# Kernel tuning notes

Hardware: AMD Instinct MI355X
Metric: run time of the kernel (lower is better)

The kernel has to match this reference:

```python
import jax, jax.numpy as jnp
import numpy as np

D_MODEL = 128
N_HEADS = 8
N_POINTS = 8
MAX_RES = 10.0


def setup_inputs() -> dict:
    key = jax.random.key(0)
    ks = jax.random.split(key, 12)
    B, C, H, W = 4, D_MODEL, 128, 128
    nh, P = N_HEADS, N_POINTS
    inp = {
        'nbr_fea': jax.random.normal(ks[0], (B, C, H, W), jnp.float32),
        'ext_fea': jax.random.normal(ks[1], (B, C, H, W), jnp.float32),
        'flow': jax.random.normal(ks[2], (B, 2, H, W), jnp.float32) * 2.0,
        'W_off': jax.random.normal(ks[3], (C, nh * P * 2), jnp.float32) * 0.02,
        'b_off': jax.random.normal(ks[4], (nh * P * 2,), jnp.float32) * 0.02,
        'W_attn': jax.random.normal(ks[5], (C, nh * P), jnp.float32) * 0.02,
        'b_attn': jnp.zeros((nh * P,), jnp.float32),
        'W_val': jax.random.normal(ks[6], (C, C), jnp.float32) * (1.0 / np.sqrt(C)),
        'b_val': jnp.zeros((C,), jnp.float32),
        'W_out': jax.random.normal(ks[7], (C, C), jnp.float32) * (1.0 / np.sqrt(C)),
        'b_out': jnp.zeros((C,), jnp.float32),
    }
    return inp


def _bilinear_gather(value, loc, H, W):
    # value: (B, nh, HW, dh)  loc: (B, nh, Q, P, 2) normalized to [0,1]
    # grid_sample semantics: align_corners=False, zero padding
    B, nh, HW, dh = value.shape
    Q, P = loc.shape[2], loc.shape[3]
    x = loc[..., 0] * W - 0.5  # (B,nh,Q,P) pixel coords
    y = loc[..., 1] * H - 0.5
    x0 = jnp.floor(x)
    y0 = jnp.floor(y)
    wx = x - x0
    wy = y - y0
    out = jnp.zeros((B, nh, Q * P, dh), value.dtype)
    for dx, dy, wgt in ((0, 0, (1 - wx) * (1 - wy)), (1, 0, wx * (1 - wy)),
                        (0, 1, (1 - wx) * wy), (1, 1, wx * wy)):
        xi = x0 + dx
        yi = y0 + dy
        valid = (xi >= 0) & (xi < W) & (yi >= 0) & (yi < H)
        xi_c = jnp.clip(xi, 0, W - 1).astype(jnp.int32)
        yi_c = jnp.clip(yi, 0, H - 1).astype(jnp.int32)
        idx = (yi_c * W + xi_c).reshape(B, nh, Q * P, 1)
        g = jnp.take_along_axis(value, idx, axis=2)  # (B,nh,QP,dh)
        w_eff = (wgt * valid.astype(value.dtype)).reshape(B, nh, Q * P, 1)
        out = out + g * w_eff
    return out.reshape(B, nh, Q, P, dh)


def reference(nbr_fea, ext_fea, flow, W_off, b_off, W_attn, b_attn, W_val, b_val, W_out, b_out):
    B, C, H, W = nbr_fea.shape
    nh, P = N_HEADS, N_POINTS
    dh = C // nh
    Q = H * W
    # normalized reference points (pixel centers / extent)
    ys = (jnp.arange(H, dtype=jnp.float32) + 0.5) / H
    xs = (jnp.arange(W, dtype=jnp.float32) + 0.5) / W
    yy, xx = jnp.meshgrid(ys, xs, indexing='ij')
    ref = jnp.stack([xx, yy], -1).reshape(Q, 2)  # (Q,2)

    ext = ext_fea.transpose(0, 2, 3, 1).reshape(B, Q, C)
    # flow-guided sampling offsets (pixels), residue bounded by tanh
    off = MAX_RES * jnp.tanh(ext @ W_off + b_off)
    off = off.reshape(B, Q, nh, P, 2)
    flow_q = flow.transpose(0, 2, 3, 1).reshape(B, Q, 1, 1, 2)
    norm = jnp.array([W, H], jnp.float32)
    loc = ref[None, :, None, None, :] + (flow_q + off) / norm  # (B,Q,nh,P,2)

    attn = jax.nn.softmax((ext @ W_attn + b_attn).reshape(B, Q, nh, P), axis=-1)

    val = (nbr_fea.transpose(0, 2, 3, 1).reshape(B, Q, C) @ W_val + b_val)
    val = val.reshape(B, Q, nh, dh).transpose(0, 2, 1, 3)  # (B,nh,HW,dh)

    sampled = _bilinear_gather(val, loc.transpose(0, 2, 1, 3, 4), H, W)  # (B,nh,Q,P,dh)
    agg = jnp.einsum('bnqpd,bqnp->bqnd', sampled, attn).reshape(B, Q, C)
    out = agg @ W_out + b_out  # (B,Q,C)
    return out.reshape(B, H, W, C).transpose(0, 3, 1, 2)
```

## Files before the change

### kernel.cpp

```cpp
#include <hip/hip_runtime.h>
#include <math.h>

namespace {
constexpr int B   = 4;
constexpr int C   = 128;
constexpr int H   = 128;
constexpr int W   = 128;
constexpr int HWn = H * W;
constexpr int NH  = 8;
}

using short8 = __attribute__((ext_vector_type(8))) short;
using f32x4  = __attribute__((ext_vector_type(4))) float;

__device__ __forceinline__ float fast_tanh(float x) {
  float e = __expf(2.f * x);
  return 1.f - 2.f / (e + 1.f);
}
__device__ __forceinline__ unsigned f2bf(float f) {
  unsigned u = __float_as_uint(f);
  return (u + 0x7FFFu + ((u >> 16) & 1u)) >> 16;
}
__device__ __forceinline__ unsigned pack2bf(float a, float b) {
  return f2bf(a) | (f2bf(b) << 16);
}

__global__ __launch_bounds__(256) void prep_weights_kernel(
    const float* __restrict__ Woff, const float* __restrict__ Wattn,
    const float* __restrict__ Wval, const float* __restrict__ Wout,
    unsigned short* __restrict__ wcat_t, unsigned short* __restrict__ wval_t,
    unsigned short* __restrict__ wout_t) {
  int row = blockIdx.x * 256 + threadIdx.x;
  if (row >= 448) return;
  const float* src; int ldn; int col; unsigned short* dst;
  if (row < 192) {
    if (row < 128) { src = Woff; ldn = 128; col = row; }
    else           { src = Wattn; ldn = 64; col = row - 128; }
    dst = wcat_t + row * 128;
  } else if (row < 320) {
    src = Wval; ldn = 128; col = row - 192; dst = wval_t + (row - 192) * 128;
  } else {
    src = Wout; ldn = 128; col = row - 320; dst = wout_t + (row - 320) * 128;
  }
  for (int k0 = 0; k0 < 128; k0 += 8) {
    unsigned pk[4];
#pragma unroll
    for (int j = 0; j < 4; ++j)
      pk[j] = pack2bf(src[(k0 + 2 * j) * ldn + col],
                      src[(k0 + 2 * j + 1) * ldn + col]);
    *(uint4*)(dst + k0) = make_uint4(pk[0], pk[1], pk[2], pk[3]);
  }
}

__global__ __launch_bounds__(256) void gemm_kernel(
    const float* __restrict__ nbr, const float* __restrict__ ext,
    const unsigned short* __restrict__ wval_t,
    const float* __restrict__ bv,
    const unsigned short* __restrict__ wcat_t,
    const float* __restrict__ boff, const float* __restrict__ battn,
    unsigned short* __restrict__ val, float* __restrict__ proj) {
  __shared__ unsigned short a_s[64 * 152];
  __shared__ unsigned short b_s[192 * 40];
  const int t    = threadIdx.x;
  const int grp  = blockIdx.x >> 10;
  const int id   = blockIdx.x & 1023;
  const int b    = id >> 8;
  const int q0   = (id & 255) * 64;
  const int wv   = t >> 6;
  const int lane = t & 63;
  const int li   = lane & 15, quad = lane >> 4;

  const float* Ab = (grp ? ext : nbr) + (size_t)b * C * HWn + q0;
#pragma unroll
  for (int it = 0; it < 4; ++it) {
    int idx = t + 256 * it;
    int kp  = idx >> 4;
    int q4  = (idx & 15) * 4;
    float4 fa = *(const float4*)(Ab + (size_t)(2 * kp) * HWn + q4);
    float4 fb = *(const float4*)(Ab + (size_t)(2 * kp + 1) * HWn + q4);
    const float* pa = &fa.x; const float* pb = &fb.x;
#pragma unroll
    for (int j = 0; j < 4; ++j)
      *(unsigned*)&a_s[(q4 + j) * 152 + 2 * kp] = pack2bf(pa[j], pb[j]);
  }

  if (grp == 0) {
    f32x4 acc[8];
#pragma unroll
    for (int n = 0; n < 8; ++n) acc[n] = (f32x4){0.f, 0.f, 0.f, 0.f};

    for (int ck = 0; ck < 4; ++ck) {
      __syncthreads();
#pragma unroll
      for (int it = 0; it < 2; ++it) {
        int idx = t + 256 * it;
        int n = idx >> 2, seg = idx & 3;
        *(uint4*)&b_s[n * 40 + seg * 8] =
            *(const uint4*)(wval_t + n * 128 + ck * 32 + seg * 8);
      }
      __syncthreads();
      short8 af = *(const short8*)&a_s[(16 * wv + li) * 152 + ck * 32 + quad * 8];
#pragma unroll
      for (int n = 0; n < 8; ++n) {
        short8 bfr = *(const short8*)&b_s[(16 * n + li) * 40 + quad * 8];
        acc[n] = __builtin_amdgcn_mfma_f32_16x16x32_bf16(af, bfr, acc[n], 0, 0, 0);
      }
    }

    __syncthreads();
#pragma unroll
    for (int n = 0; n < 8; ++n) {
      float bias = bv[16 * n + li];
#pragma unroll
      for (int reg = 0; reg < 4; ++reg) {
        int q = 16 * wv + 4 * quad + reg;
        a_s[q * 152 + 16 * n + li] = (unsigned short)f2bf(acc[n][reg] + bias);
      }
    }
    __syncthreads();
    {
      const int qi = t & 63, r = t >> 6;
      uint4 v0 = *(const uint4*)&a_s[qi * 152 + 32 * r];
      uint4 v1 = *(const uint4*)&a_s[qi * 152 + 32 * r + 8];
      uint4 v2 = *(const uint4*)&a_s[qi * 152 + 32 * r + 16];
      uint4 v3 = *(const uint4*)&a_s[qi * 152 + 32 * r + 24];
      unsigned short* d0 = val + ((size_t)(b * NH + 2 * r) * HWn + q0 + qi) * 16;
      unsigned short* d1 = val + ((size_t)(b * NH + 2 * r + 1) * HWn + q0 + qi) * 16;
      *(uint4*)d0 = v0; *(uint4*)(d0 + 8) = v1;
      *(uint4*)d1 = v2; *(uint4*)(d1 + 8) = v3;
    }
  } else {
    f32x4 acc[12];
#pragma unroll
    for (int n = 0; n < 12; ++n) acc[n] = (f32x4){0.f, 0.f, 0.f, 0.f};

    for (int ck = 0; ck < 4; ++ck) {
      __syncthreads();
#pragma unroll
      for (int it = 0; it < 3; ++it) {
        int idx = t + 256 * it;
        int n = idx >> 2, seg = idx & 3;
        *(uint4*)&b_s[n * 40 + seg * 8] =
            *(const uint4*)(wcat_t + n * 128 + ck * 32 + seg * 8);
      }
      __syncthreads();
      short8 af = *(const short8*)&a_s[(16 * wv + li) * 152 + ck * 32 + quad * 8];
#pragma unroll
      for (int n = 0; n < 12; ++n) {
        short8 bfr = *(const short8*)&b_s[(16 * n + li) * 40 + quad * 8];
        acc[n] = __builtin_amdgcn_mfma_f32_16x16x32_bf16(af, bfr, acc[n], 0, 0, 0);
      }
    }

#pragma unroll
    for (int n = 0; n < 12; ++n) {
      int col = 16 * n + li;
      float bias = (col < 128) ? boff[col] : battn[col - 128];
#pragma unroll
      for (int reg = 0; reg < 4; ++reg) {
        int q = 16 * wv + 4 * quad + reg;
        proj[(size_t)(b * HWn + q0 + q) * 192 + col] = acc[n][reg] + bias;
      }
    }
  }
}

__global__ __launch_bounds__(256) void gather_out_kernel(
    const float* __restrict__ flow, const float* __restrict__ proj,
    const unsigned short* __restrict__ val,
    const unsigned short* __restrict__ wout_t, const float* __restrict__ bout,
    float* __restrict__ out) {
  __shared__ float smem[128 * 33];
  unsigned short* a_s2 = (unsigned short*)smem;
  float* c_s = smem;

  const int t  = threadIdx.x;
  const int qi = t & 31;
  const int r  = t >> 5;

  const int blk  = blockIdx.x;
  const int lin  = (blk & 7) * 256 + (blk >> 3);
  const int b    = lin >> 9;
  const int tile = lin & 511;
  const int x0   = (tile & 7) * 16;
  const int y0   = (tile >> 3) * 2;
  const int x    = x0 + (qi & 15);
  const int y    = y0 + (qi >> 4);

  const float* pp = proj + (size_t)(b * HWn + y * W + x) * 192;
  float offa[16];
  float atta[8];
#pragma unroll
  for (int j4 = 0; j4 < 4; ++j4) {
    float4 v = *(const float4*)(pp + 16 * r + 4 * j4);
    offa[4 * j4 + 0] = 10.f * fast_tanh(v.x);
    offa[4 * j4 + 1] = 10.f * fast_tanh(v.y);
    offa[4 * j4 + 2] = 10.f * fast_tanh(v.z);
    offa[4 * j4 + 3] = 10.f * fast_tanh(v.w);
  }
#pragma unroll
  for (int j4 = 0; j4 < 2; ++j4) {
    float4 v = *(const float4*)(pp + 128 + 8 * r + 4 * j4);
    atta[4 * j4 + 0] = v.x; atta[4 * j4 + 1] = v.y;
    atta[4 * j4 + 2] = v.z; atta[4 * j4 + 3] = v.w;
  }
  {
    float m = atta[0];
#pragma unroll
    for (int p = 1; p < 8; ++p) m = fmaxf(m, atta[p]);
    float s = 0.f;
#pragma unroll
    for (int p = 0; p < 8; ++p) { float ev = __expf(atta[p] - m); atta[p] = ev; s += ev; }
    float inv = 1.f / s;
#pragma unroll
    for (int p = 0; p < 8; ++p) atta[p] *= inv;
  }

  const float xb = (float)x + flow[(size_t)b * 2 * HWn + y * W + x];
  const float yb = (float)y + flow[((size_t)b * 2 + 1) * HWn + y * W + x];

  float agg[16];
#pragma unroll
  for (int j = 0; j < 16; ++j) agg[j] = 0.f;
  const unsigned short* valh =
      val + ((size_t)b * NH + r) * HWn * 16;

#pragma unroll
  for (int p = 0; p < 8; ++p) {
    float sx = xb + offa[2 * p];
    float sy = yb + offa[2 * p + 1];
    float x0f = floorf(sx), y0f = floorf(sy);
    float wx = sx - x0f, wy = sy - y0f;
    int ix0 = (int)x0f, iy0 = (int)y0f;
    int ix1 = ix0 + 1,  iy1 = iy0 + 1;
    float aw  = atta[p];
    float w00 = aw * (1.f - wx) * (1.f - wy);
    float w10 = aw * wx * (1.f - wy);
    float w01 = aw * (1.f - wx) * wy;
    float w11 = aw * wx * wy;
    if ((unsigned)ix0 >= (unsigned)W) { w00 = 0.f; w01 = 0.f; }
    if ((unsigned)ix1 >= (unsigned)W) { w10 = 0.f; w11 = 0.f; }
    if ((unsigned)iy0 >= (unsigned)H) { w00 = 0.f; w10 = 0.f; }
    if ((unsigned)iy1 >= (unsigned)H) { w01 = 0.f; w11 = 0.f; }
    int x0c = min(max(ix0, 0), W - 1);
    int x1c = min(max(ix1, 0), W - 1);
    int y0c = min(max(iy0, 0), H - 1);
    int y1c = min(max(iy1, 0), H - 1);
    const unsigned short* c00 = valh + (size_t)(y0c * W + x0c) * 16;
    const unsigned short* c10 = valh + (size_t)(y0c * W + x1c) * 16;
    const unsigned short* c01 = valh + (size_t)(y1c * W + x0c) * 16;
    const unsigned short* c11 = valh + (size_t)(y1c * W + x1c) * 16;
#pragma unroll
    for (int cn = 0; cn < 4; ++cn) {
      const unsigned short* cp = (cn == 0) ? c00 : (cn == 1) ? c10
                                : (cn == 2) ? c01 : c11;
      float wgt = (cn == 0) ? w00 : (cn == 1) ? w10 : (cn == 2) ? w01 : w11;
      uint4 ga = ((const uint4*)cp)[0];
      uint4 gb = ((const uint4*)cp)[1];
      unsigned gs[8] = {ga.x, ga.y, ga.z, ga.w, gb.x, gb.y, gb.z, gb.w};
#pragma unroll
      for (int i = 0; i < 8; ++i) {
        float lo = __uint_as_float(gs[i] << 16);
        float hi = __uint_as_float(gs[i] & 0xFFFF0000u);
        agg[2 * i]     += wgt * lo;
        agg[2 * i + 1] += wgt * hi;
      }
    }
  }

  {
    unsigned pk[8];
#pragma unroll
    for (int j = 0; j < 8; ++j) pk[j] = pack2bf(agg[2 * j], agg[2 * j + 1]);
    uint4* dst = (uint4*)&a_s2[qi * 136 + 16 * r];
    dst[0] = make_uint4(pk[0], pk[1], pk[2], pk[3]);
    dst[1] = make_uint4(pk[4], pk[5], pk[6], pk[7]);
  }
  __syncthreads();

  const int lane = t & 63;
  const int li   = lane & 15, quad = lane >> 4;
  const int wv   = t >> 6;
  const int mt   = wv & 1;
  const int ng   = (wv >> 1) * 4;

  f32x4 acc[4];
#pragma unroll
  for (int i = 0; i < 4; ++i) acc[i] = (f32x4){0.f, 0.f, 0.f, 0.f};

#pragma unroll 1
  for (int ks = 0; ks < 4; ++ks) {
    short8 af = *(const short8*)&a_s2[(mt * 16 + li) * 136 + ks * 32 + quad * 8];
#pragma unroll
    for (int i = 0; i < 4; ++i) {
      short8 bfr = *(const short8*)(wout_t + (size_t)(16 * (ng + i) + li) * 128 +
                                    ks * 32 + quad * 8);
      acc[i] = __builtin_amdgcn_mfma_f32_16x16x32_bf16(af, bfr, acc[i], 0, 0, 0);
    }
  }
  __syncthreads();

#pragma unroll
  for (int i = 0; i < 4; ++i) {
    int c = 16 * (ng + i) + li;
    float bias = bout[c];
#pragma unroll
    for (int reg = 0; reg < 4; ++reg) {
      int q = mt * 16 + quad * 4 + reg;
      c_s[c * 33 + q] = acc[i][reg] + bias;
    }
  }
  __syncthreads();

  float* ob = out + (size_t)b * C * HWn + y * W + x;
#pragma unroll
  for (int j = 0; j < 16; ++j)
    ob[(size_t)(16 * r + j) * HWn] = c_s[(16 * r + j) * 33 + qi];
}

extern "C" void kernel_launch(void* const* d_in, const int* in_sizes, int n_in,
                              void* d_out, int out_size, void* d_ws, size_t ws_size,
                              hipStream_t stream) {
  const float* nbr   = (const float*)d_in[0];
  const float* extf  = (const float*)d_in[1];
  const float* flow  = (const float*)d_in[2];
  const float* Woff  = (const float*)d_in[3];
  const float* boff  = (const float*)d_in[4];
  const float* Wattn = (const float*)d_in[5];
  const float* battn = (const float*)d_in[6];
  const float* Wval  = (const float*)d_in[7];
  const float* bval  = (const float*)d_in[8];
  const float* Wout  = (const float*)d_in[9];
  const float* bout  = (const float*)d_in[10];
  float* outp = (float*)d_out;

  unsigned short* val    = (unsigned short*)d_ws;
  unsigned short* wcat_t = val + (size_t)B * NH * HWn * 16;
  unsigned short* wval_t = wcat_t + 192 * 128;
  unsigned short* wout_t = wval_t + 128 * 128;
  float*          proj   = (float*)(wout_t + 128 * 128);

  prep_weights_kernel<<<dim3(2), dim3(256), 0, stream>>>(
      Woff, Wattn, Wval, Wout, wcat_t, wval_t, wout_t);
  gemm_kernel<<<dim3(2048), dim3(256), 0, stream>>>(
      nbr, extf, wval_t, bval, wcat_t, boff, battn, val, proj);
  gather_out_kernel<<<dim3(2048), dim3(256), 0, stream>>>(
      flow, proj, val, wout_t, bout, outp);
}
```

Measured before the change: 223.7 us.

## Fuse offset/attention projection into gather kernel, drop proj buffer

```diff
diff --git a/kernel.cpp b/kernel.cpp
--- a/kernel.cpp
+++ b/kernel.cpp
@@ -53,24 +53,21 @@
 }
 
 __global__ __launch_bounds__(256) void gemm_kernel(
-    const float* __restrict__ nbr, const float* __restrict__ ext,
+    const float* __restrict__ nbr,
     const unsigned short* __restrict__ wval_t,
     const float* __restrict__ bv,
-    const unsigned short* __restrict__ wcat_t,
-    const float* __restrict__ boff, const float* __restrict__ battn,
-    unsigned short* __restrict__ val, float* __restrict__ proj) {
+    unsigned short* __restrict__ val) {
   __shared__ unsigned short a_s[64 * 152];
-  __shared__ unsigned short b_s[192 * 40];
+  __shared__ unsigned short b_s[128 * 40];
   const int t    = threadIdx.x;
-  const int grp  = blockIdx.x >> 10;
-  const int id   = blockIdx.x & 1023;
+  const int id   = blockIdx.x;
   const int b    = id >> 8;
   const int q0   = (id & 255) * 64;
   const int wv   = t >> 6;
   const int lane = t & 63;
   const int li   = lane & 15, quad = lane >> 4;
 
-  const float* Ab = (grp ? ext : nbr) + (size_t)b * C * HWn + q0;
+  const float* Ab = nbr + (size_t)b * C * HWn + q0;
 #pragma unroll
   for (int it = 0; it < 4; ++it) {
     int idx = t + 256 * it;
@@ -84,93 +81,62 @@
       *(unsigned*)&a_s[(q4 + j) * 152 + 2 * kp] = pack2bf(pa[j], pb[j]);
   }
 
-  if (grp == 0) {
-    f32x4 acc[8];
-#pragma unroll
-    for (int n = 0; n < 8; ++n) acc[n] = (f32x4){0.f, 0.f, 0.f, 0.f};
-
-    for (int ck = 0; ck < 4; ++ck) {
-      __syncthreads();
-#pragma unroll
-      for (int it = 0; it < 2; ++it) {
-        int idx = t + 256 * it;
-        int n = idx >> 2, seg = idx & 3;
-        *(uint4*)&b_s[n * 40 + seg * 8] =
-            *(const uint4*)(wval_t + n * 128 + ck * 32 + seg * 8);
-      }
-      __syncthreads();
-      short8 af = *(const short8*)&a_s[(16 * wv + li) * 152 + ck * 32 + quad * 8];
-#pragma unroll
-      for (int n = 0; n < 8; ++n) {
-        short8 bfr = *(const short8*)&b_s[(16 * n + li) * 40 + quad * 8];
-        acc[n] = __builtin_amdgcn_mfma_f32_16x16x32_bf16(af, bfr, acc[n], 0, 0, 0);
-      }
-    }
-
+  f32x4 acc[8];
+#pragma unroll
+  for (int n = 0; n < 8; ++n) acc[n] = (f32x4){0.f, 0.f, 0.f, 0.f};
+
+  for (int ck = 0; ck < 4; ++ck) {
     __syncthreads();
 #pragma unroll
+    for (int it = 0; it < 2; ++it) {
+      int idx = t + 256 * it;
+      int n = idx >> 2, seg = idx & 3;
+      *(uint4*)&b_s[n * 40 + seg * 8] =
+          *(const uint4*)(wval_t + n * 128 + ck * 32 + seg * 8);
+    }
+    __syncthreads();
+    short8 af = *(const short8*)&a_s[(16 * wv + li) * 152 + ck * 32 + quad * 8];
+#pragma unroll
     for (int n = 0; n < 8; ++n) {
-      float bias = bv[16 * n + li];
-#pragma unroll
-      for (int reg = 0; reg < 4; ++reg) {
-        int q = 16 * wv + 4 * quad + reg;
-        a_s[q * 152 + 16 * n + li] = (unsigned short)f2bf(acc[n][reg] + bias);
-      }
-    }
-    __syncthreads();
-    {
-      const int qi = t & 63, r = t >> 6;
-      uint4 v0 = *(const uint4*)&a_s[qi * 152 + 32 * r];
-      uint4 v1 = *(const uint4*)&a_s[qi * 152 + 32 * r + 8];
-      uint4 v2 = *(const uint4*)&a_s[qi * 152 + 32 * r + 16];
-      uint4 v3 = *(const uint4*)&a_s[qi * 152 + 32 * r + 24];
-      unsigned short* d0 = val + ((size_t)(b * NH + 2 * r) * HWn + q0 + qi) * 16;
-      unsigned short* d1 = val + ((size_t)(b * NH + 2 * r + 1) * HWn + q0 + qi) * 16;
-      *(uint4*)d0 = v0; *(uint4*)(d0 + 8) = v1;
-      *(uint4*)d1 = v2; *(uint4*)(d1 + 8) = v3;
-    }
-  } else {
-    f32x4 acc[12];
-#pragma unroll
-    for (int n = 0; n < 12; ++n) acc[n] = (f32x4){0.f, 0.f, 0.f, 0.f};
-
-    for (int ck = 0; ck < 4; ++ck) {
-      __syncthreads();
-#pragma unroll
-      for (int it = 0; it < 3; ++it) {
-        int idx = t + 256 * it;
-        int n = idx >> 2, seg = idx & 3;
-        *(uint4*)&b_s[n * 40 + seg * 8] =
-            *(const uint4*)(wcat_t + n * 128 + ck * 32 + seg * 8);
-      }
-      __syncthreads();
-      short8 af = *(const short8*)&a_s[(16 * wv + li) * 152 + ck * 32 + quad * 8];
-#pragma unroll
-      for (int n = 0; n < 12; ++n) {
-        short8 bfr = *(const short8*)&b_s[(16 * n + li) * 40 + quad * 8];
-        acc[n] = __builtin_amdgcn_mfma_f32_16x16x32_bf16(af, bfr, acc[n], 0, 0, 0);
-      }
-    }
-
-#pragma unroll
-    for (int n = 0; n < 12; ++n) {
-      int col = 16 * n + li;
-      float bias = (col < 128) ? boff[col] : battn[col - 128];
-#pragma unroll
-      for (int reg = 0; reg < 4; ++reg) {
-        int q = 16 * wv + 4 * quad + reg;
-        proj[(size_t)(b * HWn + q0 + q) * 192 + col] = acc[n][reg] + bias;
-      }
-    }
+      short8 bfr = *(const short8*)&b_s[(16 * n + li) * 40 + quad * 8];
+      acc[n] = __builtin_amdgcn_mfma_f32_16x16x32_bf16(af, bfr, acc[n], 0, 0, 0);
+    }
+  }
+
+  __syncthreads();
+#pragma unroll
+  for (int n = 0; n < 8; ++n) {
+    float bias = bv[16 * n + li];
+#pragma unroll
+    for (int reg = 0; reg < 4; ++reg) {
+      int q = 16 * wv + 4 * quad + reg;
+      a_s[q * 152 + 16 * n + li] = (unsigned short)f2bf(acc[n][reg] + bias);
+    }
+  }
+  __syncthreads();
+  {
+    const int qi = t & 63, r = t >> 6;
+    uint4 v0 = *(const uint4*)&a_s[qi * 152 + 32 * r];
+    uint4 v1 = *(const uint4*)&a_s[qi * 152 + 32 * r + 8];
+    uint4 v2 = *(const uint4*)&a_s[qi * 152 + 32 * r + 16];
+    uint4 v3 = *(const uint4*)&a_s[qi * 152 + 32 * r + 24];
+    unsigned short* d0 = val + ((size_t)(b * NH + 2 * r) * HWn + q0 + qi) * 16;
+    unsigned short* d1 = val + ((size_t)(b * NH + 2 * r + 1) * HWn + q0 + qi) * 16;
+    *(uint4*)d0 = v0; *(uint4*)(d0 + 8) = v1;
+    *(uint4*)d1 = v2; *(uint4*)(d1 + 8) = v3;
   }
 }
 
 __global__ __launch_bounds__(256) void gather_out_kernel(
-    const float* __restrict__ flow, const float* __restrict__ proj,
+    const float* __restrict__ flow, const float* __restrict__ ext,
+    const unsigned short* __restrict__ wcat_t,
+    const float* __restrict__ boff, const float* __restrict__ battn,
     const unsigned short* __restrict__ val,
     const unsigned short* __restrict__ wout_t, const float* __restrict__ bout,
     float* __restrict__ out) {
-  __shared__ float smem[128 * 33];
+  __shared__ float smem[32 * 200];
+  unsigned short* a_ext = (unsigned short*)smem;
+  float* l_s = smem;
   unsigned short* a_s2 = (unsigned short*)smem;
   float* c_s = smem;
 
@@ -187,12 +153,69 @@
   const int x    = x0 + (qi & 15);
   const int y    = y0 + (qi >> 4);
 
-  const float* pp = proj + (size_t)(b * HWn + y * W + x) * 192;
+  const int lane = t & 63;
+  const int li   = lane & 15, quad = lane >> 4;
+  const int wv   = t >> 6;
+
+  {
+    const float* Eb = ext + (size_t)b * C * HWn;
+#pragma unroll
+    for (int it = 0; it < 2; ++it) {
+      int idx = t + 256 * it;
+      int kp  = idx >> 3;
+      int pg  = idx & 7;
+      int py  = pg >> 2;
+      int xo  = (pg & 3) * 4;
+      const float* src = Eb + (size_t)(2 * kp) * HWn + (y0 + py) * W + x0 + xo;
+      float4 fa = *(const float4*)src;
+      float4 fb = *(const float4*)(src + HWn);
+      const float* pa = &fa.x; const float* pb = &fb.x;
+#pragma unroll
+      for (int j = 0; j < 4; ++j)
+        *(unsigned*)&a_ext[(pg * 4 + j) * 136 + 2 * kp] = pack2bf(pa[j], pb[j]);
+    }
+  }
+  __syncthreads();
+
+  {
+    const int mt   = wv & 1;
+    const int nset = wv >> 1;
+    f32x4 lacc[6];
+#pragma unroll
+    for (int i = 0; i < 6; ++i) lacc[i] = (f32x4){0.f, 0.f, 0.f, 0.f};
+
+#pragma unroll 1
+    for (int ks = 0; ks < 4; ++ks) {
+      short8 af = *(const short8*)&a_ext[(mt * 16 + li) * 136 + ks * 32 + quad * 8];
+#pragma unroll
+      for (int i = 0; i < 6; ++i) {
+        int n = nset * 6 + i;
+        short8 bfr = *(const short8*)(wcat_t + (size_t)(16 * n + li) * 128 +
+                                      ks * 32 + quad * 8);
+        lacc[i] = __builtin_amdgcn_mfma_f32_16x16x32_bf16(af, bfr, lacc[i], 0, 0, 0);
+      }
+    }
+    __syncthreads();
+
+#pragma unroll
+    for (int i = 0; i < 6; ++i) {
+      int col = 16 * (nset * 6 + i) + li;
+      float bias = (col < 128) ? boff[col] : battn[col - 128];
+#pragma unroll
+      for (int reg = 0; reg < 4; ++reg) {
+        int q = mt * 16 + quad * 4 + reg;
+        l_s[q * 200 + col] = lacc[i][reg] + bias;
+      }
+    }
+  }
+  __syncthreads();
+
+  const float* lrow = l_s + qi * 200;
   float offa[16];
   float atta[8];
 #pragma unroll
   for (int j4 = 0; j4 < 4; ++j4) {
-    float4 v = *(const float4*)(pp + 16 * r + 4 * j4);
+    float4 v = *(const float4*)(lrow + 16 * r + 4 * j4);
     offa[4 * j4 + 0] = 10.f * fast_tanh(v.x);
     offa[4 * j4 + 1] = 10.f * fast_tanh(v.y);
     offa[4 * j4 + 2] = 10.f * fast_tanh(v.z);
@@ -200,7 +223,7 @@
   }
 #pragma unroll
   for (int j4 = 0; j4 < 2; ++j4) {
-    float4 v = *(const float4*)(pp + 128 + 8 * r + 4 * j4);
+    float4 v = *(const float4*)(lrow + 128 + 8 * r + 4 * j4);
     atta[4 * j4 + 0] = v.x; atta[4 * j4 + 1] = v.y;
     atta[4 * j4 + 2] = v.z; atta[4 * j4 + 3] = v.w;
   }
@@ -215,6 +238,7 @@
 #pragma unroll
     for (int p = 0; p < 8; ++p) atta[p] *= inv;
   }
+  __syncthreads();
 
   const float xb = (float)x + flow[(size_t)b * 2 * HWn + y * W + x];
   const float yb = (float)y + flow[((size_t)b * 2 + 1) * HWn + y * W + x];
@@ -278,9 +302,6 @@
   }
   __syncthreads();
 
-  const int lane = t & 63;
-  const int li   = lane & 15, quad = lane >> 4;
-  const int wv   = t >> 6;
   const int mt   = wv & 1;
   const int ng   = (wv >> 1) * 4;
 
@@ -338,12 +359,11 @@
   unsigned short* wcat_t = val + (size_t)B * NH * HWn * 16;
   unsigned short* wval_t = wcat_t + 192 * 128;
   unsigned short* wout_t = wval_t + 128 * 128;
-  float*          proj   = (float*)(wout_t + 128 * 128);
 
   prep_weights_kernel<<<dim3(2), dim3(256), 0, stream>>>(
       Woff, Wattn, Wval, Wout, wcat_t, wval_t, wout_t);
-  gemm_kernel<<<dim3(2048), dim3(256), 0, stream>>>(
-      nbr, extf, wval_t, bval, wcat_t, boff, battn, val, proj);
+  gemm_kernel<<<dim3(1024), dim3(256), 0, stream>>>(
+      nbr, wval_t, bval, val);
   gather_out_kernel<<<dim3(2048), dim3(256), 0, stream>>>(
-      flow, proj, val, wout_t, bout, outp);
-}
+      flow, extf, wcat_t, boff, battn, val, wout_t, bout, outp);
+}
```

Measured after the change: 228.7 us. 2.2% more time.
